# Kernel tuning notes

Measured on AMD Instinct MI355X. Metric: run time of the kernel, lower is better.

Reference implementation:

```python
import jax, jax.numpy as jnp
import numpy as np

HIDDEN = 64
N_HEADS = 4
TOP_K = 10
ALPHA = 0.3


def setup_inputs() -> dict:
    key = jax.random.key(0)
    ks = jax.random.split(key, 12)
    B, N, T, Dd, Ds, H = 4, 2048, 32, 16, 8, HIDDEN
    s = lambda i, shape, scale: (jax.random.normal(ks[i], shape, dtype=jnp.float32) * scale)
    return {
        "x_dyn": jax.random.normal(ks[0], (B, N, T, Dd), dtype=jnp.float32),
        "x_stat": jax.random.normal(ks[1], (B, N, Ds), dtype=jnp.float32),
        "A_prior": jax.random.uniform(ks[2], (B, N, N), dtype=jnp.float32),
        "W_dyn": s(3, (Dd, H), 1.0 / np.sqrt(Dd)),
        "b_dyn": jnp.zeros((H,), jnp.float32),
        "W_stat": s(4, (Ds, H), 1.0 / np.sqrt(Ds)),
        "b_stat": jnp.zeros((H,), jnp.float32),
        "W_fuse": s(5, (2 * H, H), 1.0 / np.sqrt(2 * H)),
        "b_fuse": jnp.zeros((H,), jnp.float32),
        "Wq": s(6, (H, H), 1.0 / np.sqrt(H)),
        "Wk": s(7, (H, H), 1.0 / np.sqrt(H)),
    }


def reference(x_dyn, x_stat, A_prior, W_dyn, b_dyn, W_stat, b_stat, W_fuse, b_fuse, Wq, Wk):
    B, N = x_dyn.shape[0], x_dyn.shape[1]
    H, nh = HIDDEN, N_HEADS
    dh = H // nh

    # TemporalEncoder: linear + mean over time + ReLU -> (B, N, H)
    h = jax.nn.relu(jnp.mean(x_dyn @ W_dyn + b_dyn, axis=2))
    # FeatureEncoder: linear + ReLU -> (B, N, H)
    h_s = jax.nn.relu(x_stat @ W_stat + b_stat)
    # Fusion
    h = jnp.concatenate([h, h_s], axis=-1) @ W_fuse + b_fuse

    # GraphAttention: multi-head softmax(QK^T / sqrt(dh)) averaged over heads
    q = (h @ Wq).reshape(B, N, nh, dh)
    k = (h @ Wk).reshape(B, N, nh, dh)
    scores = jnp.einsum("bnhd,bmhd->bhnm", q, k) / jnp.sqrt(jnp.float32(dh))
    A_learn = jnp.mean(jax.nn.softmax(scores, axis=-1), axis=1)  # (B, N, N)

    # Top-k mask along last dim (scatter 1s at topk indices)
    _, topk_inds = jax.lax.top_k(A_learn, TOP_K)  # (B, N, k)
    b_idx = jnp.arange(B)[:, None, None]
    n_idx = jnp.arange(N)[None, :, None]
    mask = jnp.zeros_like(A_learn).at[b_idx, n_idx, topk_inds].set(1.0)
    A_sparse = A_learn * mask
    A_learn = (A_sparse + jnp.swapaxes(A_sparse, 1, 2)) * 0.5

    # Blend with prior
    A_final = ALPHA * A_prior + (1.0 - ALPHA) * A_learn

    # Laplacian L = D - A
    degree = jnp.sum(A_final, axis=-1)  # (B, N)
    eye = jnp.eye(N, dtype=A_final.dtype)
    L = degree[..., None] * eye - A_final
    return (L, A_final)
```

## Files before the change

### kernel.cpp

```cpp
#include <hip/hip_runtime.h>

#define NBATCH 4
#define NN 2048
#define NR 8192
#define TOPK 10
#define COLSW 2054

typedef __attribute__((ext_vector_type(4))) float f32x4;
typedef __attribute__((ext_vector_type(16))) float f32x16;
typedef __attribute__((ext_vector_type(8))) short bf16x8;

__device__ inline unsigned short f2bf(float x) {
    unsigned u = __float_as_uint(x);
    unsigned r = (u + 0x7FFF + ((u >> 16) & 1)) >> 16;
    return (unsigned short)r;
}

__global__ __launch_bounds__(256) void k1_encode(
    const float* __restrict__ xd, const float* __restrict__ xs,
    const float* __restrict__ Wd, const float* __restrict__ bd,
    const float* __restrict__ Ws, const float* __restrict__ bs,
    const float* __restrict__ Wf, const float* __restrict__ bf,
    const float* __restrict__ Wq, const float* __restrict__ Wk,
    unsigned short* __restrict__ qh, unsigned short* __restrict__ kh)
{
    int wave = threadIdx.x >> 6;
    int lane = threadIdx.x & 63;
    int r = blockIdx.x * 4 + wave;

    __shared__ float xm[4][16];
    __shared__ float xst[4][8];
    __shared__ float hc[4][128];
    __shared__ float hh[4][64];

    const float* xdr = xd + (size_t)r * 512;
    float acc = 0.f;
    #pragma unroll
    for (int j = 0; j < 8; ++j) acc += xdr[lane + 64*j];
    acc += __shfl_xor(acc, 16);
    acc += __shfl_xor(acc, 32);
    if (lane < 16) xm[wave][lane] = acc * (1.0f/32.0f);
    if (lane < 8)  xst[wave][lane] = xs[(size_t)r*8 + lane];
    __syncthreads();

    float a1 = bd[lane];
    #pragma unroll
    for (int d = 0; d < 16; ++d) a1 += xm[wave][d] * Wd[d*64 + lane];
    a1 = fmaxf(a1, 0.f);
    float a2 = bs[lane];
    #pragma unroll
    for (int d = 0; d < 8; ++d) a2 += xst[wave][d] * Ws[d*64 + lane];
    a2 = fmaxf(a2, 0.f);
    hc[wave][lane] = a1;
    hc[wave][64 + lane] = a2;
    __syncthreads();

    float hv0 = bf[lane], hv1 = 0.f, hv2 = 0.f, hv3 = 0.f;
    #pragma unroll
    for (int j = 0; j < 128; j += 4) {
        hv0 += hc[wave][j]   * Wf[(j)*64   + lane];
        hv1 += hc[wave][j+1] * Wf[(j+1)*64 + lane];
        hv2 += hc[wave][j+2] * Wf[(j+2)*64 + lane];
        hv3 += hc[wave][j+3] * Wf[(j+3)*64 + lane];
    }
    hh[wave][lane] = (hv0 + hv1) + (hv2 + hv3);
    __syncthreads();

    float qv0 = 0.f, qv1 = 0.f, kv0 = 0.f, kv1 = 0.f;
    #pragma unroll
    for (int j = 0; j < 64; j += 2) {
        float h0 = hh[wave][j], h1 = hh[wave][j+1];
        qv0 += h0 * Wq[(j)*64   + lane];
        qv1 += h1 * Wq[(j+1)*64 + lane];
        kv0 += h0 * Wk[(j)*64   + lane];
        kv1 += h1 * Wk[(j+1)*64 + lane];
    }
    float qv = qv0 + qv1, kv = kv0 + kv1;
    int b = r >> 11, n = r & 2047;
    int head = lane >> 4, dim = lane & 15;
    size_t base = ((size_t)(b*4 + head) * NN + n) * 16;
    qh[base + dim] = f2bf(qv);
    kh[base + dim] = f2bf(kv);
}

__global__ __launch_bounds__(256) void k2a_stats(
    const unsigned short* __restrict__ qh, const unsigned short* __restrict__ kh,
    float* __restrict__ Rf)
{
    const float C1 = 0.36067376022224085f;
    int bh = blockIdx.x >> 6;
    int rg = blockIdx.x & 63;
    int w = threadIdx.x >> 6, l = threadIdx.x & 63;
    int row = l & 31, khalf = l >> 5;

    bf16x8 qfrag = *(const bf16x8*)(qh + ((size_t)bh * NN + rg*32 + row) * 16 + khalf*8);
    const unsigned short* kbase = kh + (size_t)bh * NN * 16;

    __shared__ float redS[4][32];

    float Sloc = 0.f;
    for (int t = 0; t < 16; ++t) {
        int m0 = w*512 + t*32;
        bf16x8 kfrag = *(const bf16x8*)(kbase + (size_t)(m0 + row) * 16 + khalf*8);
        f32x16 acc = {0.f,0.f,0.f,0.f,0.f,0.f,0.f,0.f,0.f,0.f,0.f,0.f,0.f,0.f,0.f,0.f};
        acc = __builtin_amdgcn_mfma_f32_32x32x16_bf16(kfrag, qfrag, acc, 0, 0, 0);
        #pragma unroll
        for (int rr = 0; rr < 16; ++rr) Sloc += exp2f(acc[rr] * C1);
    }
    Sloc += __shfl_xor(Sloc, 32);
    if (l < 32) redS[w][l] = Sloc;
    __syncthreads();
    if (threadIdx.x < 32) {
        float S = redS[0][threadIdx.x] + redS[1][threadIdx.x]
                + redS[2][threadIdx.x] + redS[3][threadIdx.x];
        Rf[(size_t)bh * NN + rg*32 + threadIdx.x] = 1.0f / S;
    }
}

__global__ __launch_bounds__(256) void k3_base(
    const float* __restrict__ prior, float* __restrict__ Lout,
    float* __restrict__ Aout)
{
    int r = blockIdx.x;
    const float4* pr = (const float4*)(prior + (size_t)r * NN);
    float4* Ar = (float4*)(Aout + (size_t)r * NN);
    float4* Lr = (float4*)(Lout + (size_t)r * NN);
    float sum = 0.f;
    for (int i = threadIdx.x; i < NN/4; i += 256) {
        float4 p = pr[i];
        float4 a; a.x = 0.3f*p.x; a.y = 0.3f*p.y; a.z = 0.3f*p.z; a.w = 0.3f*p.w;
        Ar[i] = a;
        float4 lv; lv.x = -a.x; lv.y = -a.y; lv.z = -a.z; lv.w = -a.w;
        Lr[i] = lv;
        sum += a.x + a.y + a.z + a.w;
    }
    #pragma unroll
    for (int o = 32; o > 0; o >>= 1) sum += __shfl_down(sum, o);
    __shared__ float wsum[4];
    if ((threadIdx.x & 63) == 0) wsum[threadIdx.x >> 6] = sum;
    __syncthreads();
    if (threadIdx.x == 0) {
        float tot = wsum[0] + wsum[1] + wsum[2] + wsum[3];
        atomicAdd(&Lout[(size_t)r * NN + (r & 2047)], tot);
    }
}

__global__ __launch_bounds__(1024, 4) void k2b_topk(
    const unsigned short* __restrict__ qh, const unsigned short* __restrict__ kh,
    const float* __restrict__ Rf,
    float* __restrict__ Lout, float* __restrict__ Aout)
{
    const float C1 = 0.36067376022224085f;
    int b  = blockIdx.x >> 6;
    int rg = blockIdx.x & 63;
    int tid = threadIdx.x;
    int w = tid >> 6, l = tid & 63;
    int row = l & 31, khalf = l >> 5;

    __shared__ unsigned short vt[32][COLSW];

    bf16x8 qfrag[4];
    float r4[4];
    #pragma unroll
    for (int h = 0; h < 4; ++h) {
        int bh = b*4 + h;
        qfrag[h] = *(const bf16x8*)(qh + ((size_t)bh * NN + rg*32 + row) * 16 + khalf*8);
        r4[h] = Rf[(size_t)bh * NN + rg*32 + row] * 0.25f;
    }

    for (int t = 0; t < 4; ++t) {
        int m0 = w*128 + t*32;
        float vacc[16];
        #pragma unroll
        for (int rr = 0; rr < 16; ++rr) vacc[rr] = 0.f;
        #pragma unroll
        for (int h = 0; h < 4; ++h) {
            bf16x8 kfrag = *(const bf16x8*)(kh + ((size_t)(b*4+h) * NN + m0 + row) * 16 + khalf*8);
            f32x16 acc = {0.f,0.f,0.f,0.f,0.f,0.f,0.f,0.f,0.f,0.f,0.f,0.f,0.f,0.f,0.f,0.f};
            acc = __builtin_amdgcn_mfma_f32_32x32x16_bf16(kfrag, qfrag[h], acc, 0, 0, 0);
            #pragma unroll
            for (int rr = 0; rr < 16; ++rr)
                vacc[rr] = fmaf(exp2f(acc[rr] * C1), r4[h], vacc[rr]);
        }
        #pragma unroll
        for (int p = 0; p < 8; ++p) {
            int reg0 = p*2;
            int c = m0 + ((reg0 & 3) + 8*(reg0 >> 2) + 4*khalf);
            unsigned pk = (unsigned)f2bf(vacc[reg0]) | ((unsigned)f2bf(vacc[reg0+1]) << 16);
            *(unsigned*)&vt[row][c] = pk;
        }
    }
    __syncthreads();

    #pragma unroll 1
    for (int rr2 = 0; rr2 < 2; ++rr2) {
        int prow = w*2 + rr2;
        unsigned tk[TOPK];
        #pragma unroll
        for (int s = 0; s < TOPK; ++s) tk[s] = 0u;
        for (int j = 0; j < 16; ++j) {
            int m1 = 2*l + 128*j;
            unsigned pair = *(const unsigned*)&vt[prow][m1];
            unsigned key0 = (pair << 16)          | (unsigned)(2047 - m1);
            unsigned key1 = (pair & 0xFFFF0000u)  | (unsigned)(2046 - m1);
            if (key0 > tk[TOPK-1]) {
                unsigned ck = key0;
                #pragma unroll
                for (int s = 0; s < TOPK; ++s) {
                    bool ins = ck > tk[s];
                    unsigned o = tk[s];
                    tk[s] = ins ? ck : o;
                    ck    = ins ? o  : ck;
                }
            }
            if (key1 > tk[TOPK-1]) {
                unsigned ck = key1;
                #pragma unroll
                for (int s = 0; s < TOPK; ++s) {
                    bool ins = ck > tk[s];
                    unsigned o = tk[s];
                    tk[s] = ins ? ck : o;
                    ck    = ins ? o  : ck;
                }
            }
        }
        unsigned mykey = 0u;
        #pragma unroll 1
        for (int s = 0; s < TOPK; ++s) {
            unsigned kmax = tk[0];
            #pragma unroll
            for (int d = 1; d < 64; d <<= 1) {
                unsigned o = __shfl_xor(kmax, d);
                kmax = (o > kmax) ? o : kmax;
            }
            if (tk[0] == kmax) {
                #pragma unroll
                for (int q = 0; q < TOPK-1; ++q) tk[q] = tk[q+1];
                tk[TOPK-1] = 0u;
            }
            if (l == s) mykey = kmax;
        }

        if (l < TOPK) {
            float wv = 0.35f * __uint_as_float(mykey & 0xFFFF0000u);
            int j = 2047 - (int)(mykey & 0x7FFu);
            int n = rg*32 + prow;
            size_t rbase = (size_t)(b*NN + n) * NN;
            size_t jbase = (size_t)(b*NN + j) * NN;
            atomicAdd(&Aout[rbase + j],  wv);
            atomicAdd(&Aout[jbase + n],  wv);
            atomicAdd(&Lout[rbase + j], -wv);
            atomicAdd(&Lout[jbase + n], -wv);
            atomicAdd(&Lout[jbase + j],  wv);
            atomicAdd(&Lout[rbase + n],  wv);
        }
    }
}

extern "C" void kernel_launch(void* const* d_in, const int* in_sizes, int n_in,
                              void* d_out, int out_size, void* d_ws, size_t ws_size,
                              hipStream_t stream)
{
    const float* xd    = (const float*)d_in[0];
    const float* xs    = (const float*)d_in[1];
    const float* prior = (const float*)d_in[2];
    const float* Wd    = (const float*)d_in[3];
    const float* bd    = (const float*)d_in[4];
    const float* Ws    = (const float*)d_in[5];
    const float* bs    = (const float*)d_in[6];
    const float* Wf    = (const float*)d_in[7];
    const float* bf    = (const float*)d_in[8];
    const float* Wq    = (const float*)d_in[9];
    const float* Wk    = (const float*)d_in[10];

    float* Lout = (float*)d_out;
    float* Aout = Lout + (size_t)NR * NN;

    unsigned short* qh = (unsigned short*)d_ws;
    unsigned short* kh = qh + (size_t)16 * NN * 16;
    float* Rf  = (float*)(kh + (size_t)16 * NN * 16);

    k1_encode<<<NR/4, 256, 0, stream>>>(xd, xs, Wd, bd, Ws, bs, Wf, bf, Wq, Wk, qh, kh);
    k2a_stats<<<16*64, 256, 0, stream>>>(qh, kh, Rf);
    k3_base<<<NR, 256, 0, stream>>>(prior, Lout, Aout);
    k2b_topk<<<NBATCH*64, 1024, 0, stream>>>(qh, kh, Rf, Lout, Aout);
}
```

Baseline: 328.5 us.

## Replace scattered global atomics with CSR bucketing and single fused output pass

Instead of writing the prior-scaled base matrices first and then scattering six global float atomics per top-k winner into L and A, top-k winners are recorded in a buffer and counted per row. A scan and placement kernel build a CSR list of contributions per row. A final per-row kernel loads the prior, accumulates the sparse entries in shared memory, and writes A and L once, including the degree on the diagonal. This removes random global atomics and the read-modify-write of the outputs, at the cost of two extra small launches, including a single-block scan.

```diff
diff --git a/kernel.cpp b/kernel.cpp
--- a/kernel.cpp
+++ b/kernel.cpp
@@ -6,7 +6,6 @@
 #define TOPK 10
 #define COLSW 2054
 
-typedef __attribute__((ext_vector_type(4))) float f32x4;
 typedef __attribute__((ext_vector_type(16))) float f32x16;
 typedef __attribute__((ext_vector_type(8))) short bf16x8;
 
@@ -22,8 +21,11 @@
     const float* __restrict__ Ws, const float* __restrict__ bs,
     const float* __restrict__ Wf, const float* __restrict__ bf,
     const float* __restrict__ Wq, const float* __restrict__ Wk,
-    unsigned short* __restrict__ qh, unsigned short* __restrict__ kh)
-{
+    unsigned short* __restrict__ qh, unsigned short* __restrict__ kh,
+    unsigned* __restrict__ cnt)
+{
+    if (blockIdx.x < 32) cnt[blockIdx.x * 256 + threadIdx.x] = 0u;
+
     int wave = threadIdx.x >> 6;
     int lane = threadIdx.x & 63;
     int r = blockIdx.x * 4 + wave;
@@ -117,38 +119,10 @@
     }
 }
 
-__global__ __launch_bounds__(256) void k3_base(
-    const float* __restrict__ prior, float* __restrict__ Lout,
-    float* __restrict__ Aout)
-{
-    int r = blockIdx.x;
-    const float4* pr = (const float4*)(prior + (size_t)r * NN);
-    float4* Ar = (float4*)(Aout + (size_t)r * NN);
-    float4* Lr = (float4*)(Lout + (size_t)r * NN);
-    float sum = 0.f;
-    for (int i = threadIdx.x; i < NN/4; i += 256) {
-        float4 p = pr[i];
-        float4 a; a.x = 0.3f*p.x; a.y = 0.3f*p.y; a.z = 0.3f*p.z; a.w = 0.3f*p.w;
-        Ar[i] = a;
-        float4 lv; lv.x = -a.x; lv.y = -a.y; lv.z = -a.z; lv.w = -a.w;
-        Lr[i] = lv;
-        sum += a.x + a.y + a.z + a.w;
-    }
-    #pragma unroll
-    for (int o = 32; o > 0; o >>= 1) sum += __shfl_down(sum, o);
-    __shared__ float wsum[4];
-    if ((threadIdx.x & 63) == 0) wsum[threadIdx.x >> 6] = sum;
-    __syncthreads();
-    if (threadIdx.x == 0) {
-        float tot = wsum[0] + wsum[1] + wsum[2] + wsum[3];
-        atomicAdd(&Lout[(size_t)r * NN + (r & 2047)], tot);
-    }
-}
-
 __global__ __launch_bounds__(1024, 4) void k2b_topk(
     const unsigned short* __restrict__ qh, const unsigned short* __restrict__ kh,
     const float* __restrict__ Rf,
-    float* __restrict__ Lout, float* __restrict__ Aout)
+    unsigned long long* __restrict__ winners, unsigned* __restrict__ cnt)
 {
     const float C1 = 0.36067376022224085f;
     int b  = blockIdx.x >> 6;
@@ -241,19 +215,110 @@
             if (l == s) mykey = kmax;
         }
 
+        int n = rg*32 + prow;
+        int r = b*NN + n;
+        if (l == 0) atomicAdd(&cnt[r], (unsigned)TOPK);
         if (l < TOPK) {
             float wv = 0.35f * __uint_as_float(mykey & 0xFFFF0000u);
-            int j = 2047 - (int)(mykey & 0x7FFu);
-            int n = rg*32 + prow;
-            size_t rbase = (size_t)(b*NN + n) * NN;
-            size_t jbase = (size_t)(b*NN + j) * NN;
-            atomicAdd(&Aout[rbase + j],  wv);
-            atomicAdd(&Aout[jbase + n],  wv);
-            atomicAdd(&Lout[rbase + j], -wv);
-            atomicAdd(&Lout[jbase + n], -wv);
-            atomicAdd(&Lout[jbase + j],  wv);
-            atomicAdd(&Lout[rbase + n],  wv);
-        }
+            unsigned j = 2047u - (mykey & 0x7FFu);
+            unsigned rj = (unsigned)(b*NN) + j;
+            atomicAdd(&cnt[rj], 1u);
+            winners[(size_t)r * TOPK + l] =
+                ((unsigned long long)__float_as_uint(wv) << 32)
+                | ((unsigned)r << 11) | j;
+        }
+    }
+}
+
+__global__ __launch_bounds__(1024) void kscan(
+    const unsigned* __restrict__ cnt,
+    unsigned* __restrict__ row_ptr, unsigned* __restrict__ cursor)
+{
+    int t = threadIdx.x;
+    unsigned loc[8]; unsigned s = 0u;
+    #pragma unroll
+    for (int i = 0; i < 8; ++i) { loc[i] = s; s += cnt[t*8 + i]; }
+    __shared__ unsigned ss[1024];
+    ss[t] = s;
+    __syncthreads();
+    for (int off = 1; off < 1024; off <<= 1) {
+        unsigned v = (t >= off) ? ss[t - off] : 0u;
+        __syncthreads();
+        ss[t] += v;
+        __syncthreads();
+    }
+    unsigned base = ss[t] - s;
+    #pragma unroll
+    for (int i = 0; i < 8; ++i) {
+        unsigned v = base + loc[i];
+        row_ptr[t*8 + i] = v;
+        cursor[t*8 + i]  = v;
+    }
+}
+
+__global__ __launch_bounds__(256) void kplace(
+    const unsigned long long* __restrict__ winners,
+    unsigned* __restrict__ cursor, unsigned long long* __restrict__ entries)
+{
+    int idx = blockIdx.x * 256 + threadIdx.x;
+    unsigned long long wp = winners[idx];
+    unsigned lo = (unsigned)wp;
+    unsigned r  = (lo >> 11) & 8191u;
+    unsigned j  = lo & 2047u;
+    unsigned long long hv = wp & 0xFFFFFFFF00000000ull;
+    unsigned rj = (r & ~2047u) | j;
+    unsigned s1 = atomicAdd(&cursor[r], 1u);
+    entries[s1] = hv | j;
+    unsigned s2 = atomicAdd(&cursor[rj], 1u);
+    entries[s2] = hv | (r & 2047u);
+}
+
+__global__ __launch_bounds__(256) void k3_final(
+    const float* __restrict__ prior,
+    const unsigned* __restrict__ row_ptr, const unsigned* __restrict__ cnt,
+    const unsigned long long* __restrict__ entries,
+    float* __restrict__ Lout, float* __restrict__ Aout)
+{
+    int r = blockIdx.x;
+    int tid = threadIdx.x;
+    __shared__ float arow[NN];
+    __shared__ float wsum[4];
+    __shared__ float esum;
+    if (tid == 0) esum = 0.f;
+
+    const float4* pr = (const float4*)(prior + (size_t)r * NN);
+    float sum = 0.f;
+    for (int i = tid; i < NN/4; i += 256) {
+        float4 p = pr[i];
+        float4 a; a.x = 0.3f*p.x; a.y = 0.3f*p.y; a.z = 0.3f*p.z; a.w = 0.3f*p.w;
+        *(float4*)&arow[4*i] = a;
+        sum += a.x + a.y + a.z + a.w;
+    }
+    #pragma unroll
+    for (int o = 32; o > 0; o >>= 1) sum += __shfl_down(sum, o);
+    if ((tid & 63) == 0) wsum[tid >> 6] = sum;
+    __syncthreads();
+
+    unsigned c0 = cnt[r], st = row_ptr[r];
+    for (unsigned t = tid; t < c0; t += 256) {
+        unsigned long long e = entries[st + t];
+        float wv = __uint_as_float((unsigned)(e >> 32));
+        unsigned col = (unsigned)e & 2047u;
+        atomicAdd(&arow[col], wv);
+        atomicAdd(&esum, wv);
+    }
+    __syncthreads();
+
+    float deg = wsum[0] + wsum[1] + wsum[2] + wsum[3] + esum;
+    int diag = r & 2047;
+    float4* Ar = (float4*)(Aout + (size_t)r * NN);
+    float4* Lr = (float4*)(Lout + (size_t)r * NN);
+    for (int i = tid; i < NN/4; i += 256) {
+        float4 a = *(const float4*)&arow[4*i];
+        Ar[i] = a;
+        float4 lv; lv.x = -a.x; lv.y = -a.y; lv.z = -a.z; lv.w = -a.w;
+        if (i == (diag >> 2)) ((float*)&lv)[diag & 3] += deg;
+        Lr[i] = lv;
     }
 }
 
@@ -279,9 +344,16 @@
     unsigned short* qh = (unsigned short*)d_ws;
     unsigned short* kh = qh + (size_t)16 * NN * 16;
     float* Rf  = (float*)(kh + (size_t)16 * NN * 16);
-
-    k1_encode<<<NR/4, 256, 0, stream>>>(xd, xs, Wd, bd, Ws, bs, Wf, bf, Wq, Wk, qh, kh);
+    unsigned* cnt     = (unsigned*)(Rf + (size_t)16 * NN);
+    unsigned* row_ptr = cnt + NR;
+    unsigned* cursor  = row_ptr + NR;
+    unsigned long long* winners = (unsigned long long*)(cursor + NR);
+    unsigned long long* entries = winners + (size_t)TOPK * NR;
+
+    k1_encode<<<NR/4, 256, 0, stream>>>(xd, xs, Wd, bd, Ws, bs, Wf, bf, Wq, Wk, qh, kh, cnt);
     k2a_stats<<<16*64, 256, 0, stream>>>(qh, kh, Rf);
-    k3_base<<<NR, 256, 0, stream>>>(prior, Lout, Aout);
-    k2b_topk<<<NBATCH*64, 1024, 0, stream>>>(qh, kh, Rf, Lout, Aout);
-}
+    k2b_topk<<<NBATCH*64, 1024, 0, stream>>>(qh, kh, Rf, winners, cnt);
+    kscan<<<1, 1024, 0, stream>>>(cnt, row_ptr, cursor);
+    kplace<<<TOPK*NR/256, 256, 0, stream>>>(winners, cursor, entries);
+    k3_final<<<NR, 256, 0, stream>>>(prior, row_ptr, cnt, entries, Lout, Aout);
+}
```

After: 337.9 us. 1.03x slower.

## Fuse softmax row-sum pass into top-k kernel and merge diagonal atomics

Applied to the files above, without the earlier changes.

Removes the separate stats kernel. The fused top-k kernel now computes the per-head softmax denominators itself with an extra MFMA+exp pass over all keys, reduced through shared memory, and then recomputes scores for the top-k pass. This saves a kernel launch and the Rf workspace round-trip, but the main kernel's compute roughly doubles and it runs on only 256 blocks, where the old stats kernel used 1024 blocks. It also sums the ten diagonal Laplacian contributions with a wave shuffle so each row issues one atomic to that address instead of ten.

```diff
diff --git a/kernel.cpp b/kernel.cpp
--- a/kernel.cpp
+++ b/kernel.cpp
@@ -6,7 +6,6 @@
 #define TOPK 10
 #define COLSW 2054
 
-typedef __attribute__((ext_vector_type(4))) float f32x4;
 typedef __attribute__((ext_vector_type(16))) float f32x16;
 typedef __attribute__((ext_vector_type(8))) short bf16x8;
 
@@ -81,40 +80,6 @@
     size_t base = ((size_t)(b*4 + head) * NN + n) * 16;
     qh[base + dim] = f2bf(qv);
     kh[base + dim] = f2bf(kv);
-}
-
-__global__ __launch_bounds__(256) void k2a_stats(
-    const unsigned short* __restrict__ qh, const unsigned short* __restrict__ kh,
-    float* __restrict__ Rf)
-{
-    const float C1 = 0.36067376022224085f;
-    int bh = blockIdx.x >> 6;
-    int rg = blockIdx.x & 63;
-    int w = threadIdx.x >> 6, l = threadIdx.x & 63;
-    int row = l & 31, khalf = l >> 5;
-
-    bf16x8 qfrag = *(const bf16x8*)(qh + ((size_t)bh * NN + rg*32 + row) * 16 + khalf*8);
-    const unsigned short* kbase = kh + (size_t)bh * NN * 16;
-
-    __shared__ float redS[4][32];
-
-    float Sloc = 0.f;
-    for (int t = 0; t < 16; ++t) {
-        int m0 = w*512 + t*32;
-        bf16x8 kfrag = *(const bf16x8*)(kbase + (size_t)(m0 + row) * 16 + khalf*8);
-        f32x16 acc = {0.f,0.f,0.f,0.f,0.f,0.f,0.f,0.f,0.f,0.f,0.f,0.f,0.f,0.f,0.f,0.f};
-        acc = __builtin_amdgcn_mfma_f32_32x32x16_bf16(kfrag, qfrag, acc, 0, 0, 0);
-        #pragma unroll
-        for (int rr = 0; rr < 16; ++rr) Sloc += exp2f(acc[rr] * C1);
-    }
-    Sloc += __shfl_xor(Sloc, 32);
-    if (l < 32) redS[w][l] = Sloc;
-    __syncthreads();
-    if (threadIdx.x < 32) {
-        float S = redS[0][threadIdx.x] + redS[1][threadIdx.x]
-                + redS[2][threadIdx.x] + redS[3][threadIdx.x];
-        Rf[(size_t)bh * NN + rg*32 + threadIdx.x] = 1.0f / S;
-    }
 }
 
 __global__ __launch_bounds__(256) void k3_base(
@@ -145,9 +110,8 @@
     }
 }
 
-__global__ __launch_bounds__(1024, 4) void k2b_topk(
+__global__ __launch_bounds__(1024, 4) void k2_fused(
     const unsigned short* __restrict__ qh, const unsigned short* __restrict__ kh,
-    const float* __restrict__ Rf,
     float* __restrict__ Lout, float* __restrict__ Aout)
 {
     const float C1 = 0.36067376022224085f;
@@ -158,15 +122,45 @@
     int row = l & 31, khalf = l >> 5;
 
     __shared__ unsigned short vt[32][COLSW];
+    __shared__ float redS[16][4][32];
+    __shared__ float r4s[4][32];
 
     bf16x8 qfrag[4];
+    #pragma unroll
+    for (int h = 0; h < 4; ++h)
+        qfrag[h] = *(const bf16x8*)(qh + ((size_t)(b*4+h) * NN + rg*32 + row) * 16 + khalf*8);
+
+    float Sl[4] = {0.f, 0.f, 0.f, 0.f};
+    for (int t = 0; t < 4; ++t) {
+        int m0 = w*128 + t*32;
+        #pragma unroll
+        for (int h = 0; h < 4; ++h) {
+            bf16x8 kfrag = *(const bf16x8*)(kh + ((size_t)(b*4+h) * NN + m0 + row) * 16 + khalf*8);
+            f32x16 acc = {0.f,0.f,0.f,0.f,0.f,0.f,0.f,0.f,0.f,0.f,0.f,0.f,0.f,0.f,0.f,0.f};
+            acc = __builtin_amdgcn_mfma_f32_32x32x16_bf16(kfrag, qfrag[h], acc, 0, 0, 0);
+            #pragma unroll
+            for (int rr = 0; rr < 16; ++rr) Sl[h] += exp2f(acc[rr] * C1);
+        }
+    }
+    #pragma unroll
+    for (int h = 0; h < 4; ++h) Sl[h] += __shfl_xor(Sl[h], 32);
+    if (l < 32) {
+        #pragma unroll
+        for (int h = 0; h < 4; ++h) redS[w][h][l] = Sl[h];
+    }
+    __syncthreads();
+    if (tid < 128) {
+        int h = tid >> 5, rw = tid & 31;
+        float s = 0.f;
+        #pragma unroll
+        for (int ww = 0; ww < 16; ++ww) s += redS[ww][h][rw];
+        r4s[h][rw] = 0.25f / s;
+    }
+    __syncthreads();
+
     float r4[4];
     #pragma unroll
-    for (int h = 0; h < 4; ++h) {
-        int bh = b*4 + h;
-        qfrag[h] = *(const bf16x8*)(qh + ((size_t)bh * NN + rg*32 + row) * 16 + khalf*8);
-        r4[h] = Rf[(size_t)bh * NN + rg*32 + row] * 0.25f;
-    }
+    for (int h = 0; h < 4; ++h) r4[h] = r4s[h][row];
 
     for (int t = 0; t < 4; ++t) {
         int m0 = w*128 + t*32;
@@ -241,18 +235,25 @@
             if (l == s) mykey = kmax;
         }
 
+        int n = rg*32 + prow;
+        size_t rbase = (size_t)(b*NN + n) * NN;
+        float wv = 0.f;
+        int j = 0;
         if (l < TOPK) {
-            float wv = 0.35f * __uint_as_float(mykey & 0xFFFF0000u);
-            int j = 2047 - (int)(mykey & 0x7FFu);
-            int n = rg*32 + prow;
-            size_t rbase = (size_t)(b*NN + n) * NN;
+            wv = 0.35f * __uint_as_float(mykey & 0xFFFF0000u);
+            j = 2047 - (int)(mykey & 0x7FFu);
+        }
+        float swv = wv;
+        #pragma unroll
+        for (int d = 1; d <= 8; d <<= 1) swv += __shfl_xor(swv, d);
+        if (l == 0) atomicAdd(&Lout[rbase + n], swv);
+        if (l < TOPK) {
             size_t jbase = (size_t)(b*NN + j) * NN;
             atomicAdd(&Aout[rbase + j],  wv);
             atomicAdd(&Aout[jbase + n],  wv);
             atomicAdd(&Lout[rbase + j], -wv);
             atomicAdd(&Lout[jbase + n], -wv);
             atomicAdd(&Lout[jbase + j],  wv);
-            atomicAdd(&Lout[rbase + n],  wv);
         }
     }
 }
@@ -278,10 +279,8 @@
 
     unsigned short* qh = (unsigned short*)d_ws;
     unsigned short* kh = qh + (size_t)16 * NN * 16;
-    float* Rf  = (float*)(kh + (size_t)16 * NN * 16);
 
     k1_encode<<<NR/4, 256, 0, stream>>>(xd, xs, Wd, bd, Ws, bs, Wf, bf, Wq, Wk, qh, kh);
-    k2a_stats<<<16*64, 256, 0, stream>>>(qh, kh, Rf);
     k3_base<<<NR, 256, 0, stream>>>(prior, Lout, Aout);
-    k2b_topk<<<NBATCH*64, 1024, 0, stream>>>(qh, kh, Rf, Lout, Aout);
-}
+    k2_fused<<<NBATCH*64, 1024, 0, stream>>>(qh, kh, Lout, Aout);
+}
```

Measured after the change: 322.3 us. Within noise of the previous version (-1.9%).
